# Kernel tuning notes

Hardware: AMD Instinct MI355X
Metric: run time of the kernel (lower is better)

## Reference

```python
import jax, jax.numpy as jnp
import numpy as np

N_NODES = 50000
N_EDGES = 800000
IN_FEATS = 128
OUT_FEATS = 128


def setup_inputs() -> dict:
    key = jax.random.key(0)
    k1, k2, k3, k4 = jax.random.split(key, 4)
    x = jax.random.normal(k1, (N_NODES, IN_FEATS), dtype=jnp.float32)
    src = jax.random.randint(k2, (N_EDGES,), 0, N_NODES, dtype=jnp.int32)
    dst = jax.random.randint(k3, (N_EDGES,), 0, N_NODES, dtype=jnp.int32)
    # xavier_uniform init for weight [in_feats, out_feats]
    limit = float(np.sqrt(6.0 / (IN_FEATS + OUT_FEATS)))
    weight = jax.random.uniform(k4, (IN_FEATS, OUT_FEATS), dtype=jnp.float32,
                                minval=-limit, maxval=limit)
    bias = jnp.zeros((OUT_FEATS,), dtype=jnp.float32)
    return {"x": x, "src": src, "dst": dst, "weight": weight, "bias": bias}


def reference(x, src, dst, weight, bias):
    # GraphConv, norm='both', no edge_weight (copy_u path), single partition:
    #   x <- x * out_deg^{-1/2}
    #   h[v] = sum_{(u->v) in E} x[u]            (SpMM aggregation)
    #   rst = h @ W                               (GEMM)
    #   rst <- rst * in_deg^{-1/2} + bias
    n = x.shape[0]
    ones = jnp.ones(src.shape[0], dtype=x.dtype)
    deg_out = jax.ops.segment_sum(ones, src, num_segments=n)     # [N]
    deg_out = jnp.maximum(deg_out, 1.0)[:, None]                  # clamp(min=1)
    xn = x * jax.lax.rsqrt(deg_out)                               # left norm
    h = jax.ops.segment_sum(xn[src], dst, num_segments=n)        # [N, in]
    rst = h @ weight                                              # [N, out]
    deg_in = jax.ops.segment_sum(ones, dst, num_segments=n)      # [N]
    deg_in = jnp.maximum(deg_in, 1.0)[:, None]
    rst = rst * jax.lax.rsqrt(deg_in)                             # right norm
    return rst + bias
```

## Files before the change

### kernel.cpp

```cpp
#include <hip/hip_runtime.h>

#define F 128
#define RANGE 12500
#define WT_LD 136

typedef unsigned short ushort_t;
typedef _Float16 half8 __attribute__((ext_vector_type(8)));
typedef float f32x4 __attribute__((ext_vector_type(4)));

__device__ inline float bf_lo(unsigned u) { return __uint_as_float(u << 16); }
__device__ inline float bf_hi(unsigned u) { return __uint_as_float(u & 0xffff0000u); }
__device__ inline ushort_t f2bf(float f) {
    unsigned u = __float_as_uint(f);
    return (ushort_t)((u + 0x7fff + ((u >> 16) & 1)) >> 16);
}

__global__ __launch_bounds__(256)
void hist_both_kernel(const int* __restrict__ src, const int* __restrict__ dst,
                      int* __restrict__ part, int E, int S, int SLICE) {
    __shared__ int h[RANGE];
    int b = blockIdx.x, t = threadIdx.x;
    int r = b / S, s = b % S;
    int lo = r * RANGE;
    for (int i = t; i < RANGE; i += 256) h[i] = 0;
    __syncthreads();
    int e0 = s * SLICE, e1 = min(e0 + SLICE, E);
    int e = e0 + t * 4;
    for (; e + 3 < e1; e += 1024) {
        int4 vs4 = *(const int4*)(src + e);
        int4 vd4 = *(const int4*)(dst + e);
        int vs, vd;
        vs = vs4.x - lo; if ((unsigned)vs < (unsigned)RANGE) atomicAdd(&h[vs], 1);
        vs = vs4.y - lo; if ((unsigned)vs < (unsigned)RANGE) atomicAdd(&h[vs], 1);
        vs = vs4.z - lo; if ((unsigned)vs < (unsigned)RANGE) atomicAdd(&h[vs], 1);
        vs = vs4.w - lo; if ((unsigned)vs < (unsigned)RANGE) atomicAdd(&h[vs], 1);
        vd = vd4.x - lo; if ((unsigned)vd < (unsigned)RANGE) atomicAdd(&h[vd], 0x10000);
        vd = vd4.y - lo; if ((unsigned)vd < (unsigned)RANGE) atomicAdd(&h[vd], 0x10000);
        vd = vd4.z - lo; if ((unsigned)vd < (unsigned)RANGE) atomicAdd(&h[vd], 0x10000);
        vd = vd4.w - lo; if ((unsigned)vd < (unsigned)RANGE) atomicAdd(&h[vd], 0x10000);
    }
    for (; e < e1; ++e) {
        int vs = src[e] - lo;
        int vd = dst[e] - lo;
        if ((unsigned)vs < (unsigned)RANGE) atomicAdd(&h[vs], 1);
        if ((unsigned)vd < (unsigned)RANGE) atomicAdd(&h[vd], 0x10000);
    }
    __syncthreads();
    int* outp = part + (size_t)b * RANGE;
    for (int i = t; i < RANGE; i += 256) outp[i] = h[i];
}

__global__ __launch_bounds__(256)
void reduce_all_kernel(const int* __restrict__ part, ushort_t* __restrict__ pre16,
                       float* __restrict__ inv_out, int* __restrict__ cnt_in,
                       int* __restrict__ psum, int S, int N) {
    int b = blockIdx.x, t = threadIdx.x;
    int v = b * 256 + t;
    int run = 0;
    if (v < N) {
        int r = v / RANGE, vp = v % RANGE;
        const int* p = part + (size_t)r * S * RANGE + vp;
        ushort_t* q = pre16 + (size_t)r * S * RANGE + vp;
        int sum_s = 0;
        for (int s = 0; s < S; ++s) {
            int tv = p[(size_t)s * RANGE];
            sum_s += tv & 0xffff;
            q[(size_t)s * RANGE] = (ushort_t)run;
            run += (tv >> 16);
        }
        inv_out[v] = rsqrtf(fmaxf((float)sum_s, 1.0f));
        cnt_in[v] = run;
    }
    int bl = run;
    #pragma unroll
    for (int off = 32; off > 0; off >>= 1) bl += __shfl_down(bl, off);
    __shared__ int ws[4];
    int lane = t & 63, w = t >> 6;
    if (lane == 0) ws[w] = bl;
    __syncthreads();
    if (t == 0) psum[b] = ws[0] + ws[1] + ws[2] + ws[3];
}

__global__ __launch_bounds__(256)
void scan_rows_kernel(const int* __restrict__ cnt_in, const int* __restrict__ psum,
                      int* __restrict__ row_off, int N, int E, int NP) {
    int b = blockIdx.x, t = threadIdx.x;
    int pv = (t < 4 * b && t < NP) ? psum[t] : 0;
    #pragma unroll
    for (int off = 32; off > 0; off >>= 1) pv += __shfl_down(pv, off);
    __shared__ int red[4];
    int lane = t & 63, w = t >> 6;
    if (lane == 0) red[w] = pv;
    if (b == 0 && t == 0) row_off[N] = E;
    __syncthreads();
    int base = red[0] + red[1] + red[2] + red[3];

    int i0 = b * 1024 + t * 4;
    int v[4]; int s = 0;
    #pragma unroll
    for (int j = 0; j < 4; ++j) { int i = i0 + j; v[j] = (i < N) ? cnt_in[i] : 0; s += v[j]; }
    int incl = s;
    #pragma unroll
    for (int off = 1; off < 64; off <<= 1) {
        int u = __shfl_up(incl, off);
        if (lane >= off) incl += u;
    }
    __shared__ int wsum[4];
    if (lane == 63) wsum[w] = incl;
    __syncthreads();
    int wbase = 0;
    #pragma unroll
    for (int j = 0; j < 4; ++j) if (j < w) wbase += wsum[j];
    int run = base + wbase + (incl - s);
    #pragma unroll
    for (int j = 0; j < 4; ++j) {
        int i = i0 + j;
        if (i < N) { row_off[i] = run; run += v[j]; }
    }
}

__global__ __launch_bounds__(256)
void fill_kernel(const int* __restrict__ src, const int* __restrict__ dst,
                 const int* __restrict__ row_off, const ushort_t* __restrict__ pre16,
                 ushort_t* __restrict__ csr_src, int E, int S, int SLICE, int N) {
    __shared__ int cur[RANGE];
    int b = blockIdx.x, t = threadIdx.x;
    int r = b / S, s = b % S;
    int lo = r * RANGE;
    int hi = min(lo + RANGE, N);
    const ushort_t* pp = pre16 + (size_t)b * RANGE;
    for (int i = t; i < hi - lo; i += 256) cur[i] = row_off[lo + i] + pp[i];
    __syncthreads();
    int e0 = s * SLICE, e1 = min(e0 + SLICE, E);
    int e = e0 + t * 4;
    for (; e + 3 < e1; e += 1024) {
        int4 vd4 = *(const int4*)(dst + e);
        int4 vs4 = *(const int4*)(src + e);
        int d;
        d = vd4.x - lo; if ((unsigned)d < (unsigned)(hi - lo)) { int pos = atomicAdd(&cur[d], 1); csr_src[pos] = (ushort_t)vs4.x; }
        d = vd4.y - lo; if ((unsigned)d < (unsigned)(hi - lo)) { int pos = atomicAdd(&cur[d], 1); csr_src[pos] = (ushort_t)vs4.y; }
        d = vd4.z - lo; if ((unsigned)d < (unsigned)(hi - lo)) { int pos = atomicAdd(&cur[d], 1); csr_src[pos] = (ushort_t)vs4.z; }
        d = vd4.w - lo; if ((unsigned)d < (unsigned)(hi - lo)) { int pos = atomicAdd(&cur[d], 1); csr_src[pos] = (ushort_t)vs4.w; }
    }
    for (; e < e1; ++e) {
        int d = dst[e] - lo;
        if ((unsigned)d < (unsigned)(hi - lo)) {
            int pos = atomicAdd(&cur[d], 1);
            csr_src[pos] = (ushort_t)src[e];
        }
    }
}

__global__ __launch_bounds__(256)
void gemm_kernel(const float* __restrict__ x, const float* __restrict__ W,
                 const float* __restrict__ inv_out, ushort_t* __restrict__ Y, int N) {
    __shared__ _Float16 Wt[128 * WT_LD];
    const int t = threadIdx.x;
    for (int i = t; i < 128 * 128; i += 256) {
        int k = i >> 7, c = i & 127;
        Wt[c * WT_LD + k] = (_Float16)W[i];
    }
    __syncthreads();

    const int wv = t >> 6;
    const int l  = t & 63;
    const int m  = l & 15;
    const int q  = l >> 4;
    const int r0w = blockIdx.x * 64 + wv * 16;
    const int rowload = min(r0w + m, N - 1);
    const float* xr = x + (size_t)rowload * F;

    f32x4 acc[8] = {};
    #pragma unroll
    for (int k0 = 0; k0 < 128; k0 += 32) {
        const int kk = k0 + q * 8;
        float4 xa = *(const float4*)(xr + kk);
        float4 xb = *(const float4*)(xr + kk + 4);
        half8 a;
        a[0] = (_Float16)xa.x; a[1] = (_Float16)xa.y;
        a[2] = (_Float16)xa.z; a[3] = (_Float16)xa.w;
        a[4] = (_Float16)xb.x; a[5] = (_Float16)xb.y;
        a[6] = (_Float16)xb.z; a[7] = (_Float16)xb.w;
        #pragma unroll
        for (int ct = 0; ct < 8; ++ct) {
            half8 bfr = *(const half8*)&Wt[(ct * 16 + m) * WT_LD + kk];
            acc[ct] = __builtin_amdgcn_mfma_f32_16x16x32_f16(a, bfr, acc[ct], 0, 0, 0);
        }
    }

    float sc[4]; int rvalid[4];
    #pragma unroll
    for (int reg = 0; reg < 4; ++reg) {
        int rr = r0w + q * 4 + reg;
        rvalid[reg] = rr < N;
        sc[reg] = inv_out[min(rr, N - 1)];
    }
    #pragma unroll
    for (int ct = 0; ct < 8; ++ct) {
        #pragma unroll
        for (int reg = 0; reg < 4; ++reg) {
            if (rvalid[reg]) {
                int rr = r0w + q * 4 + reg;
                Y[(size_t)rr * F + ct * 16 + m] = f2bf(acc[ct][reg] * sc[reg]);
            }
        }
    }
}

__global__ __launch_bounds__(256)
void gather_kernel(const ushort_t* __restrict__ Y, const ushort_t* __restrict__ csr_src,
                   const int* __restrict__ row_off, const float* __restrict__ bias,
                   float* __restrict__ out, int N) {
    int v = blockIdx.x * 4 + (threadIdx.x >> 6);
    if (v >= N) return;
    int lane = threadIdx.x & 63;
    int q = lane >> 4;
    int l16 = lane & 15;
    int beg = row_off[v], end = row_off[v + 1];
    float aA[8] = {0,0,0,0,0,0,0,0};
    float aB[8] = {0,0,0,0,0,0,0,0};
    float aC[8] = {0,0,0,0,0,0,0,0};
    float aD[8] = {0,0,0,0,0,0,0,0};
    int j = beg + q;
    for (; j + 12 < end; j += 16) {
        int s0 = csr_src[j];
        int s1 = csr_src[j + 4];
        int s2 = csr_src[j + 8];
        int s3 = csr_src[j + 12];
        uint4 u0 = *(const uint4*)(Y + (size_t)s0 * F + l16 * 8);
        uint4 u1 = *(const uint4*)(Y + (size_t)s1 * F + l16 * 8);
        uint4 u2 = *(const uint4*)(Y + (size_t)s2 * F + l16 * 8);
        uint4 u3 = *(const uint4*)(Y + (size_t)s3 * F + l16 * 8);
        aA[0] += bf_lo(u0.x); aA[1] += bf_hi(u0.x);
        aA[2] += bf_lo(u0.y); aA[3] += bf_hi(u0.y);
        aA[4] += bf_lo(u0.z); aA[5] += bf_hi(u0.z);
        aA[6] += bf_lo(u0.w); aA[7] += bf_hi(u0.w);
        aB[0] += bf_lo(u1.x); aB[1] += bf_hi(u1.x);
        aB[2] += bf_lo(u1.y); aB[3] += bf_hi(u1.y);
        aB[4] += bf_lo(u1.z); aB[5] += bf_hi(u1.z);
        aB[6] += bf_lo(u1.w); aB[7] += bf_hi(u1.w);
        aC[0] += bf_lo(u2.x); aC[1] += bf_hi(u2.x);
        aC[2] += bf_lo(u2.y); aC[3] += bf_hi(u2.y);
        aC[4] += bf_lo(u2.z); aC[5] += bf_hi(u2.z);
        aC[6] += bf_lo(u2.w); aC[7] += bf_hi(u2.w);
        aD[0] += bf_lo(u3.x); aD[1] += bf_hi(u3.x);
        aD[2] += bf_lo(u3.y); aD[3] += bf_hi(u3.y);
        aD[4] += bf_lo(u3.z); aD[5] += bf_hi(u3.z);
        aD[6] += bf_lo(u3.w); aD[7] += bf_hi(u3.w);
    }
    for (; j < end; j += 4) {
        int s0 = csr_src[j];
        uint4 u0 = *(const uint4*)(Y + (size_t)s0 * F + l16 * 8);
        aA[0] += bf_lo(u0.x); aA[1] += bf_hi(u0.x);
        aA[2] += bf_lo(u0.y); aA[3] += bf_hi(u0.y);
        aA[4] += bf_lo(u0.z); aA[5] += bf_hi(u0.z);
        aA[6] += bf_lo(u0.w); aA[7] += bf_hi(u0.w);
    }
    #pragma unroll
    for (int i = 0; i < 8; ++i) {
        float a = (aA[i] + aB[i]) + (aC[i] + aD[i]);
        a += __shfl_xor(a, 16);
        a += __shfl_xor(a, 32);
        aA[i] = a;
    }
    if (q == 0) {
        float invd = rsqrtf(fmaxf((float)(end - beg), 1.0f));
        float4 b0 = *(const float4*)(bias + l16 * 8);
        float4 b1 = *(const float4*)(bias + l16 * 8 + 4);
        float4 o0, o1;
        o0.x = aA[0] * invd + b0.x; o0.y = aA[1] * invd + b0.y;
        o0.z = aA[2] * invd + b0.z; o0.w = aA[3] * invd + b0.w;
        o1.x = aA[4] * invd + b1.x; o1.y = aA[5] * invd + b1.y;
        o1.z = aA[6] * invd + b1.z; o1.w = aA[7] * invd + b1.w;
        *(float4*)(out + (size_t)v * F + l16 * 8) = o0;
        *(float4*)(out + (size_t)v * F + l16 * 8 + 4) = o1;
    }
}

extern "C" void kernel_launch(void* const* d_in, const int* in_sizes, int n_in,
                              void* d_out, int out_size, void* d_ws, size_t ws_size,
                              hipStream_t stream) {
    const float* x    = (const float*)d_in[0];
    const int*   src  = (const int*)d_in[1];
    const int*   dst  = (const int*)d_in[2];
    const float* W    = (const float*)d_in[3];
    const float* bias = (const float*)d_in[4];
    float* out = (float*)d_out;

    const int N = in_sizes[0] / F;
    const int E = in_sizes[1];
    const int NB = (N + 1023) / 1024;
    const int NP = (N + 255) / 256;
    const int R = (N + RANGE - 1) / RANGE;

    size_t fixed_words = (size_t)N + (size_t)(N + 1) + (size_t)N + (size_t)NP
                       + (size_t)(E + 1) / 2 + 128
                       + ((size_t)N * F + 1) / 2 + 128;
    int S = 64;
    while (S > 2 && (fixed_words + (size_t)R * S * RANGE * 3 / 2) * 4 > ws_size) S >>= 1;
    const int SLICE = (E + S - 1) / S;

    int*   part    = (int*)d_ws;
    int*   cnt_in  = part + (size_t)R * S * RANGE;
    int*   row_off = cnt_in + N;
    float* inv_out = (float*)(row_off + N + 1);
    int*   psum    = (int*)(inv_out + N);
    size_t off_w   = ((size_t)(psum + NP - (int*)d_ws) + 63) & ~(size_t)63;
    ushort_t* csr_src = (ushort_t*)((int*)d_ws + off_w);
    size_t off_w2  = (off_w + ((size_t)E + 1) / 2 + 63) & ~(size_t)63;
    ushort_t* Y    = (ushort_t*)((int*)d_ws + off_w2);
    size_t off_w3  = (off_w2 + ((size_t)N * F + 1) / 2 + 63) & ~(size_t)63;
    ushort_t* pre16 = (ushort_t*)((int*)d_ws + off_w3);

    const int hgrid = R * S;

    hist_both_kernel<<<hgrid, 256, 0, stream>>>(src, dst, part, E, S, SLICE);
    reduce_all_kernel<<<NP, 256, 0, stream>>>(part, pre16, inv_out, cnt_in, psum, S, N);
    scan_rows_kernel<<<NB, 256, 0, stream>>>(cnt_in, psum, row_off, N, E, NP);
    fill_kernel<<<hgrid, 256, 0, stream>>>(src, dst, row_off, pre16, csr_src, E, S, SLICE, N);
    gemm_kernel<<<(N + 63) / 64, 256, 0, stream>>>(x, W, inv_out, Y, N);
    gather_kernel<<<(N + 3) / 4, 256, 0, stream>>>(Y, csr_src, row_off, bias, out, N);
}
```

Before: 174.9 us.

## Replace sliced shared-memory histograms with global atomics and fuse CSR fill into GEMM

Replaces the partitioned shared-memory histogram, reduce and per-slice prefix pipeline with one global-atomic degree kernel, a single scan kernel that also computes the out-degree norms, and a CSR fill that runs as extra blocks of the GEMM launch. The fill increments the row offsets in place, so the gather reads the row end from ro[v] and the row start from ro[v-1]. This removes the large per-slice partial buffers, the extra passes over them and two launches, and lets the scatter overlap the GEMM. In exchange it relies on global atomics with no ordering within a row, and the gather tail now handles up to three leftover edges per lane group.

Result: slower. 250.6 us (+43.3%).

```diff
diff --git a/kernel.cpp b/kernel.cpp
--- a/kernel.cpp
+++ b/kernel.cpp
@@ -1,7 +1,6 @@
 #include <hip/hip_runtime.h>
 
 #define F 128
-#define RANGE 12500
 #define WT_LD 136
 
 typedef unsigned short ushort_t;
@@ -16,89 +15,77 @@
 }
 
 __global__ __launch_bounds__(256)
-void hist_both_kernel(const int* __restrict__ src, const int* __restrict__ dst,
-                      int* __restrict__ part, int E, int S, int SLICE) {
-    __shared__ int h[RANGE];
+void zero_kernel(int* __restrict__ deg, int N) {
+    int i = (blockIdx.x * 256 + threadIdx.x) * 4;
+    if (i + 3 < N) {
+        *(int4*)(deg + i) = make_int4(0, 0, 0, 0);
+    } else {
+        for (; i < N; ++i) deg[i] = 0;
+    }
+}
+
+__global__ __launch_bounds__(256)
+void deg_kernel(const int* __restrict__ src, const int* __restrict__ dst,
+                int* __restrict__ deg, int E) {
+    int i = (blockIdx.x * 256 + threadIdx.x) * 4;
+    if (i + 3 < E) {
+        int4 s4 = *(const int4*)(src + i);
+        int4 d4 = *(const int4*)(dst + i);
+        atomicAdd(&deg[s4.x], 1);
+        atomicAdd(&deg[s4.y], 1);
+        atomicAdd(&deg[s4.z], 1);
+        atomicAdd(&deg[s4.w], 1);
+        atomicAdd(&deg[d4.x], 0x10000);
+        atomicAdd(&deg[d4.y], 0x10000);
+        atomicAdd(&deg[d4.z], 0x10000);
+        atomicAdd(&deg[d4.w], 0x10000);
+    } else {
+        for (; i < E; ++i) {
+            atomicAdd(&deg[src[i]], 1);
+            atomicAdd(&deg[dst[i]], 0x10000);
+        }
+    }
+}
+
+__global__ __launch_bounds__(256)
+void scan_kernel(const int* __restrict__ deg, float* __restrict__ inv_out,
+                 int* __restrict__ ro, int N) {
     int b = blockIdx.x, t = threadIdx.x;
-    int r = b / S, s = b % S;
-    int lo = r * RANGE;
-    for (int i = t; i < RANGE; i += 256) h[i] = 0;
+    int lane = t & 63, w = t >> 6;
+    int lim = b << 10;
+
+    int acc = 0;
+    for (int i = t * 4; i < lim; i += 1024) {
+        int4 d4 = *(const int4*)(deg + i);
+        acc += (int)(((unsigned)d4.x >> 16) + ((unsigned)d4.y >> 16)
+                   + ((unsigned)d4.z >> 16) + ((unsigned)d4.w >> 16));
+    }
+    #pragma unroll
+    for (int off = 32; off > 0; off >>= 1) acc += __shfl_down(acc, off);
+    __shared__ int bsum[4];
+    if (lane == 0) bsum[w] = acc;
     __syncthreads();
-    int e0 = s * SLICE, e1 = min(e0 + SLICE, E);
-    int e = e0 + t * 4;
-    for (; e + 3 < e1; e += 1024) {
-        int4 vs4 = *(const int4*)(src + e);
-        int4 vd4 = *(const int4*)(dst + e);
-        int vs, vd;
-        vs = vs4.x - lo; if ((unsigned)vs < (unsigned)RANGE) atomicAdd(&h[vs], 1);
-        vs = vs4.y - lo; if ((unsigned)vs < (unsigned)RANGE) atomicAdd(&h[vs], 1);
-        vs = vs4.z - lo; if ((unsigned)vs < (unsigned)RANGE) atomicAdd(&h[vs], 1);
-        vs = vs4.w - lo; if ((unsigned)vs < (unsigned)RANGE) atomicAdd(&h[vs], 1);
-        vd = vd4.x - lo; if ((unsigned)vd < (unsigned)RANGE) atomicAdd(&h[vd], 0x10000);
-        vd = vd4.y - lo; if ((unsigned)vd < (unsigned)RANGE) atomicAdd(&h[vd], 0x10000);
-        vd = vd4.z - lo; if ((unsigned)vd < (unsigned)RANGE) atomicAdd(&h[vd], 0x10000);
-        vd = vd4.w - lo; if ((unsigned)vd < (unsigned)RANGE) atomicAdd(&h[vd], 0x10000);
-    }
-    for (; e < e1; ++e) {
-        int vs = src[e] - lo;
-        int vd = dst[e] - lo;
-        if ((unsigned)vs < (unsigned)RANGE) atomicAdd(&h[vs], 1);
-        if ((unsigned)vd < (unsigned)RANGE) atomicAdd(&h[vd], 0x10000);
-    }
-    __syncthreads();
-    int* outp = part + (size_t)b * RANGE;
-    for (int i = t; i < RANGE; i += 256) outp[i] = h[i];
-}
-
-__global__ __launch_bounds__(256)
-void reduce_all_kernel(const int* __restrict__ part, ushort_t* __restrict__ pre16,
-                       float* __restrict__ inv_out, int* __restrict__ cnt_in,
-                       int* __restrict__ psum, int S, int N) {
-    int b = blockIdx.x, t = threadIdx.x;
-    int v = b * 256 + t;
-    int run = 0;
-    if (v < N) {
-        int r = v / RANGE, vp = v % RANGE;
-        const int* p = part + (size_t)r * S * RANGE + vp;
-        ushort_t* q = pre16 + (size_t)r * S * RANGE + vp;
-        int sum_s = 0;
-        for (int s = 0; s < S; ++s) {
-            int tv = p[(size_t)s * RANGE];
-            sum_s += tv & 0xffff;
-            q[(size_t)s * RANGE] = (ushort_t)run;
-            run += (tv >> 16);
-        }
-        inv_out[v] = rsqrtf(fmaxf((float)sum_s, 1.0f));
-        cnt_in[v] = run;
-    }
-    int bl = run;
-    #pragma unroll
-    for (int off = 32; off > 0; off >>= 1) bl += __shfl_down(bl, off);
-    __shared__ int ws[4];
-    int lane = t & 63, w = t >> 6;
-    if (lane == 0) ws[w] = bl;
-    __syncthreads();
-    if (t == 0) psum[b] = ws[0] + ws[1] + ws[2] + ws[3];
-}
-
-__global__ __launch_bounds__(256)
-void scan_rows_kernel(const int* __restrict__ cnt_in, const int* __restrict__ psum,
-                      int* __restrict__ row_off, int N, int E, int NP) {
-    int b = blockIdx.x, t = threadIdx.x;
-    int pv = (t < 4 * b && t < NP) ? psum[t] : 0;
-    #pragma unroll
-    for (int off = 32; off > 0; off >>= 1) pv += __shfl_down(pv, off);
-    __shared__ int red[4];
-    int lane = t & 63, w = t >> 6;
-    if (lane == 0) red[w] = pv;
-    if (b == 0 && t == 0) row_off[N] = E;
-    __syncthreads();
-    int base = red[0] + red[1] + red[2] + red[3];
-
-    int i0 = b * 1024 + t * 4;
-    int v[4]; int s = 0;
-    #pragma unroll
-    for (int j = 0; j < 4; ++j) { int i = i0 + j; v[j] = (i < N) ? cnt_in[i] : 0; s += v[j]; }
+    int base = bsum[0] + bsum[1] + bsum[2] + bsum[3];
+
+    int i0 = lim + t * 4;
+    int v4[4]; int s = 0;
+    if (i0 < N) {
+        int4 d4 = *(const int4*)(deg + i0);
+        v4[0] = (int)((unsigned)d4.x >> 16);
+        v4[1] = (int)((unsigned)d4.y >> 16);
+        v4[2] = (int)((unsigned)d4.z >> 16);
+        v4[3] = (int)((unsigned)d4.w >> 16);
+        s = v4[0] + v4[1] + v4[2] + v4[3];
+        float4 iv;
+        iv.x = rsqrtf(fmaxf((float)(d4.x & 0xffff), 1.0f));
+        iv.y = rsqrtf(fmaxf((float)(d4.y & 0xffff), 1.0f));
+        iv.z = rsqrtf(fmaxf((float)(d4.z & 0xffff), 1.0f));
+        iv.w = rsqrtf(fmaxf((float)(d4.w & 0xffff), 1.0f));
+        *(float4*)(inv_out + i0) = iv;
+    } else {
+        v4[0] = v4[1] = v4[2] = v4[3] = 0;
+    }
+
     int incl = s;
     #pragma unroll
     for (int off = 1; off < 64; off <<= 1) {
@@ -112,50 +99,46 @@
     #pragma unroll
     for (int j = 0; j < 4; ++j) if (j < w) wbase += wsum[j];
     int run = base + wbase + (incl - s);
-    #pragma unroll
-    for (int j = 0; j < 4; ++j) {
-        int i = i0 + j;
-        if (i < N) { row_off[i] = run; run += v[j]; }
-    }
-}
-
-__global__ __launch_bounds__(256)
-void fill_kernel(const int* __restrict__ src, const int* __restrict__ dst,
-                 const int* __restrict__ row_off, const ushort_t* __restrict__ pre16,
-                 ushort_t* __restrict__ csr_src, int E, int S, int SLICE, int N) {
-    __shared__ int cur[RANGE];
-    int b = blockIdx.x, t = threadIdx.x;
-    int r = b / S, s = b % S;
-    int lo = r * RANGE;
-    int hi = min(lo + RANGE, N);
-    const ushort_t* pp = pre16 + (size_t)b * RANGE;
-    for (int i = t; i < hi - lo; i += 256) cur[i] = row_off[lo + i] + pp[i];
-    __syncthreads();
-    int e0 = s * SLICE, e1 = min(e0 + SLICE, E);
-    int e = e0 + t * 4;
-    for (; e + 3 < e1; e += 1024) {
-        int4 vd4 = *(const int4*)(dst + e);
-        int4 vs4 = *(const int4*)(src + e);
-        int d;
-        d = vd4.x - lo; if ((unsigned)d < (unsigned)(hi - lo)) { int pos = atomicAdd(&cur[d], 1); csr_src[pos] = (ushort_t)vs4.x; }
-        d = vd4.y - lo; if ((unsigned)d < (unsigned)(hi - lo)) { int pos = atomicAdd(&cur[d], 1); csr_src[pos] = (ushort_t)vs4.y; }
-        d = vd4.z - lo; if ((unsigned)d < (unsigned)(hi - lo)) { int pos = atomicAdd(&cur[d], 1); csr_src[pos] = (ushort_t)vs4.z; }
-        d = vd4.w - lo; if ((unsigned)d < (unsigned)(hi - lo)) { int pos = atomicAdd(&cur[d], 1); csr_src[pos] = (ushort_t)vs4.w; }
-    }
-    for (; e < e1; ++e) {
-        int d = dst[e] - lo;
-        if ((unsigned)d < (unsigned)(hi - lo)) {
-            int pos = atomicAdd(&cur[d], 1);
-            csr_src[pos] = (ushort_t)src[e];
-        }
-    }
-}
-
-__global__ __launch_bounds__(256)
-void gemm_kernel(const float* __restrict__ x, const float* __restrict__ W,
-                 const float* __restrict__ inv_out, ushort_t* __restrict__ Y, int N) {
+    if (i0 < N) {
+        int4 r4;
+        r4.x = run; run += v4[0];
+        r4.y = run; run += v4[1];
+        r4.z = run; run += v4[2];
+        r4.w = run;
+        *(int4*)(ro + i0) = r4;
+    }
+}
+
+__global__ __launch_bounds__(256)
+void gemm_fill_kernel(const float* __restrict__ x, const float* __restrict__ W,
+                      const float* __restrict__ inv_out, ushort_t* __restrict__ Y,
+                      const int* __restrict__ src, const int* __restrict__ dst,
+                      int* __restrict__ ro, ushort_t* __restrict__ csr,
+                      int N, int E, int FB) {
     __shared__ _Float16 Wt[128 * WT_LD];
     const int t = threadIdx.x;
+    const int blk = blockIdx.x;
+
+    if (blk < FB) {
+        int i = (blk * 256 + t) * 4;
+        if (i + 3 < E) {
+            int4 d4 = *(const int4*)(dst + i);
+            int4 s4 = *(const int4*)(src + i);
+            int p;
+            p = atomicAdd(&ro[d4.x], 1); csr[p] = (ushort_t)s4.x;
+            p = atomicAdd(&ro[d4.y], 1); csr[p] = (ushort_t)s4.y;
+            p = atomicAdd(&ro[d4.z], 1); csr[p] = (ushort_t)s4.z;
+            p = atomicAdd(&ro[d4.w], 1); csr[p] = (ushort_t)s4.w;
+        } else {
+            for (; i < E; ++i) {
+                int p = atomicAdd(&ro[dst[i]], 1);
+                csr[p] = (ushort_t)src[i];
+            }
+        }
+        return;
+    }
+
+    const int gb = blk - FB;
     for (int i = t; i < 128 * 128; i += 256) {
         int k = i >> 7, c = i & 127;
         Wt[c * WT_LD + k] = (_Float16)W[i];
@@ -166,7 +149,7 @@
     const int l  = t & 63;
     const int m  = l & 15;
     const int q  = l >> 4;
-    const int r0w = blockIdx.x * 64 + wv * 16;
+    const int r0w = gb * 64 + wv * 16;
     const int rowload = min(r0w + m, N - 1);
     const float* xr = x + (size_t)rowload * F;
 
@@ -208,25 +191,26 @@
 }
 
 __global__ __launch_bounds__(256)
-void gather_kernel(const ushort_t* __restrict__ Y, const ushort_t* __restrict__ csr_src,
-                   const int* __restrict__ row_off, const float* __restrict__ bias,
+void gather_kernel(const ushort_t* __restrict__ Y, const ushort_t* __restrict__ csr,
+                   const int* __restrict__ ro, const float* __restrict__ bias,
                    float* __restrict__ out, int N) {
     int v = blockIdx.x * 4 + (threadIdx.x >> 6);
     if (v >= N) return;
     int lane = threadIdx.x & 63;
     int q = lane >> 4;
     int l16 = lane & 15;
-    int beg = row_off[v], end = row_off[v + 1];
+    int end = ro[v];
+    int beg = (v == 0) ? 0 : ro[v - 1];
     float aA[8] = {0,0,0,0,0,0,0,0};
     float aB[8] = {0,0,0,0,0,0,0,0};
     float aC[8] = {0,0,0,0,0,0,0,0};
     float aD[8] = {0,0,0,0,0,0,0,0};
     int j = beg + q;
     for (; j + 12 < end; j += 16) {
-        int s0 = csr_src[j];
-        int s1 = csr_src[j + 4];
-        int s2 = csr_src[j + 8];
-        int s3 = csr_src[j + 12];
+        int s0 = csr[j];
+        int s1 = csr[j + 4];
+        int s2 = csr[j + 8];
+        int s3 = csr[j + 12];
         uint4 u0 = *(const uint4*)(Y + (size_t)s0 * F + l16 * 8);
         uint4 u1 = *(const uint4*)(Y + (size_t)s1 * F + l16 * 8);
         uint4 u2 = *(const uint4*)(Y + (size_t)s2 * F + l16 * 8);
@@ -248,13 +232,29 @@
         aD[4] += bf_lo(u3.z); aD[5] += bf_hi(u3.z);
         aD[6] += bf_lo(u3.w); aD[7] += bf_hi(u3.w);
     }
-    for (; j < end; j += 4) {
-        int s0 = csr_src[j];
+    if (j < end) {
+        int s0 = csr[j];
         uint4 u0 = *(const uint4*)(Y + (size_t)s0 * F + l16 * 8);
         aA[0] += bf_lo(u0.x); aA[1] += bf_hi(u0.x);
         aA[2] += bf_lo(u0.y); aA[3] += bf_hi(u0.y);
         aA[4] += bf_lo(u0.z); aA[5] += bf_hi(u0.z);
         aA[6] += bf_lo(u0.w); aA[7] += bf_hi(u0.w);
+    }
+    if (j + 4 < end) {
+        int s1 = csr[j + 4];
+        uint4 u1 = *(const uint4*)(Y + (size_t)s1 * F + l16 * 8);
+        aB[0] += bf_lo(u1.x); aB[1] += bf_hi(u1.x);
+        aB[2] += bf_lo(u1.y); aB[3] += bf_hi(u1.y);
+        aB[4] += bf_lo(u1.z); aB[5] += bf_hi(u1.z);
+        aB[6] += bf_lo(u1.w); aB[7] += bf_hi(u1.w);
+    }
+    if (j + 8 < end) {
+        int s2 = csr[j + 8];
+        uint4 u2 = *(const uint4*)(Y + (size_t)s2 * F + l16 * 8);
+        aC[0] += bf_lo(u2.x); aC[1] += bf_hi(u2.x);
+        aC[2] += bf_lo(u2.y); aC[3] += bf_hi(u2.y);
+        aC[4] += bf_lo(u2.z); aC[5] += bf_hi(u2.z);
+        aC[6] += bf_lo(u2.w); aC[7] += bf_hi(u2.w);
     }
     #pragma unroll
     for (int i = 0; i < 8; ++i) {
@@ -289,35 +289,24 @@
 
     const int N = in_sizes[0] / F;
     const int E = in_sizes[1];
-    const int NB = (N + 1023) / 1024;
-    const int NP = (N + 255) / 256;
-    const int R = (N + RANGE - 1) / RANGE;
-
-    size_t fixed_words = (size_t)N + (size_t)(N + 1) + (size_t)N + (size_t)NP
-                       + (size_t)(E + 1) / 2 + 128
-                       + ((size_t)N * F + 1) / 2 + 128;
-    int S = 64;
-    while (S > 2 && (fixed_words + (size_t)R * S * RANGE * 3 / 2) * 4 > ws_size) S >>= 1;
-    const int SLICE = (E + S - 1) / S;
-
-    int*   part    = (int*)d_ws;
-    int*   cnt_in  = part + (size_t)R * S * RANGE;
-    int*   row_off = cnt_in + N;
-    float* inv_out = (float*)(row_off + N + 1);
-    int*   psum    = (int*)(inv_out + N);
-    size_t off_w   = ((size_t)(psum + NP - (int*)d_ws) + 63) & ~(size_t)63;
-    ushort_t* csr_src = (ushort_t*)((int*)d_ws + off_w);
-    size_t off_w2  = (off_w + ((size_t)E + 1) / 2 + 63) & ~(size_t)63;
-    ushort_t* Y    = (ushort_t*)((int*)d_ws + off_w2);
-    size_t off_w3  = (off_w2 + ((size_t)N * F + 1) / 2 + 63) & ~(size_t)63;
-    ushort_t* pre16 = (ushort_t*)((int*)d_ws + off_w3);
-
-    const int hgrid = R * S;
-
-    hist_both_kernel<<<hgrid, 256, 0, stream>>>(src, dst, part, E, S, SLICE);
-    reduce_all_kernel<<<NP, 256, 0, stream>>>(part, pre16, inv_out, cnt_in, psum, S, N);
-    scan_rows_kernel<<<NB, 256, 0, stream>>>(cnt_in, psum, row_off, N, E, NP);
-    fill_kernel<<<hgrid, 256, 0, stream>>>(src, dst, row_off, pre16, csr_src, E, S, SLICE, N);
-    gemm_kernel<<<(N + 63) / 64, 256, 0, stream>>>(x, W, inv_out, Y, N);
-    gather_kernel<<<(N + 3) / 4, 256, 0, stream>>>(Y, csr_src, row_off, bias, out, N);
-}
+
+    int*   deg     = (int*)d_ws;
+    int*   ro      = deg + N;
+    float* inv_out = (float*)(ro + N);
+    size_t csr_off = (size_t)N * 12;
+    ushort_t* csr  = (ushort_t*)((char*)d_ws + csr_off);
+    size_t y_off   = (csr_off + (size_t)E * 2 + 255) & ~(size_t)255;
+    ushort_t* Y    = (ushort_t*)((char*)d_ws + y_off);
+
+    const int ZB = (N + 1023) / 1024;
+    const int EB = (E + 1023) / 1024;
+    const int SB = (N + 1023) / 1024;
+    const int GB = (N + 63) / 64;
+
+    zero_kernel<<<ZB, 256, 0, stream>>>(deg, N);
+    deg_kernel<<<EB, 256, 0, stream>>>(src, dst, deg, E);
+    scan_kernel<<<SB, 256, 0, stream>>>(deg, inv_out, ro, N);
+    gemm_fill_kernel<<<EB + GB, 256, 0, stream>>>(x, W, inv_out, Y, src, dst,
+                                                  ro, csr, N, E, EB);
+    gather_kernel<<<(N + 3) / 4, 256, 0, stream>>>(Y, csr, ro, bias, out, N);
+}
```

## Merge CSR fill and GEMM into one launch; unroll gather tail

Applied to the files above, without the earlier changes.

The CSR fill kernel and the GEMM kernel are independent, so they are merged into one launch whose first blocks do the fill and whose remaining blocks do the GEMM, with shared memory as a union. This removes one kernel boundary and lets the atomic-bound fill and the MFMA-bound GEMM run at the same time on different CUs. The gather tail loop is replaced by up to three predicated loads feeding separate accumulators, which adds more loads in flight. The union takes the larger of the two shared-memory footprints, which can lower occupancy for the GEMM blocks.

New measurement: 167.0 us. -4.5%, faster.

```diff
diff --git a/kernel.cpp b/kernel.cpp
--- a/kernel.cpp
+++ b/kernel.cpp
@@ -120,45 +120,51 @@
 }
 
 __global__ __launch_bounds__(256)
-void fill_kernel(const int* __restrict__ src, const int* __restrict__ dst,
-                 const int* __restrict__ row_off, const ushort_t* __restrict__ pre16,
-                 ushort_t* __restrict__ csr_src, int E, int S, int SLICE, int N) {
-    __shared__ int cur[RANGE];
-    int b = blockIdx.x, t = threadIdx.x;
-    int r = b / S, s = b % S;
-    int lo = r * RANGE;
-    int hi = min(lo + RANGE, N);
-    const ushort_t* pp = pre16 + (size_t)b * RANGE;
-    for (int i = t; i < hi - lo; i += 256) cur[i] = row_off[lo + i] + pp[i];
-    __syncthreads();
-    int e0 = s * SLICE, e1 = min(e0 + SLICE, E);
-    int e = e0 + t * 4;
-    for (; e + 3 < e1; e += 1024) {
-        int4 vd4 = *(const int4*)(dst + e);
-        int4 vs4 = *(const int4*)(src + e);
-        int d;
-        d = vd4.x - lo; if ((unsigned)d < (unsigned)(hi - lo)) { int pos = atomicAdd(&cur[d], 1); csr_src[pos] = (ushort_t)vs4.x; }
-        d = vd4.y - lo; if ((unsigned)d < (unsigned)(hi - lo)) { int pos = atomicAdd(&cur[d], 1); csr_src[pos] = (ushort_t)vs4.y; }
-        d = vd4.z - lo; if ((unsigned)d < (unsigned)(hi - lo)) { int pos = atomicAdd(&cur[d], 1); csr_src[pos] = (ushort_t)vs4.z; }
-        d = vd4.w - lo; if ((unsigned)d < (unsigned)(hi - lo)) { int pos = atomicAdd(&cur[d], 1); csr_src[pos] = (ushort_t)vs4.w; }
-    }
-    for (; e < e1; ++e) {
-        int d = dst[e] - lo;
-        if ((unsigned)d < (unsigned)(hi - lo)) {
-            int pos = atomicAdd(&cur[d], 1);
-            csr_src[pos] = (ushort_t)src[e];
-        }
-    }
-}
-
-__global__ __launch_bounds__(256)
-void gemm_kernel(const float* __restrict__ x, const float* __restrict__ W,
-                 const float* __restrict__ inv_out, ushort_t* __restrict__ Y, int N) {
-    __shared__ _Float16 Wt[128 * WT_LD];
+void fill_gemm_kernel(const int* __restrict__ src, const int* __restrict__ dst,
+                      const int* __restrict__ row_off, const ushort_t* __restrict__ pre16,
+                      ushort_t* __restrict__ csr_src,
+                      const float* __restrict__ x, const float* __restrict__ W,
+                      const float* __restrict__ inv_out, ushort_t* __restrict__ Y,
+                      int E, int S, int SLICE, int N, int FB) {
+    __shared__ union {
+        int cur[RANGE];
+        _Float16 Wt[128 * WT_LD];
+    } sm;
     const int t = threadIdx.x;
+    const int blk = blockIdx.x;
+
+    if (blk < FB) {
+        int r = blk / S, s = blk % S;
+        int lo = r * RANGE;
+        int hi = min(lo + RANGE, N);
+        const ushort_t* pp = pre16 + (size_t)blk * RANGE;
+        for (int i = t; i < hi - lo; i += 256) sm.cur[i] = row_off[lo + i] + pp[i];
+        __syncthreads();
+        int e0 = s * SLICE, e1 = min(e0 + SLICE, E);
+        int e = e0 + t * 4;
+        for (; e + 3 < e1; e += 1024) {
+            int4 vd4 = *(const int4*)(dst + e);
+            int4 vs4 = *(const int4*)(src + e);
+            int d;
+            d = vd4.x - lo; if ((unsigned)d < (unsigned)(hi - lo)) { int pos = atomicAdd(&sm.cur[d], 1); csr_src[pos] = (ushort_t)vs4.x; }
+            d = vd4.y - lo; if ((unsigned)d < (unsigned)(hi - lo)) { int pos = atomicAdd(&sm.cur[d], 1); csr_src[pos] = (ushort_t)vs4.y; }
+            d = vd4.z - lo; if ((unsigned)d < (unsigned)(hi - lo)) { int pos = atomicAdd(&sm.cur[d], 1); csr_src[pos] = (ushort_t)vs4.z; }
+            d = vd4.w - lo; if ((unsigned)d < (unsigned)(hi - lo)) { int pos = atomicAdd(&sm.cur[d], 1); csr_src[pos] = (ushort_t)vs4.w; }
+        }
+        for (; e < e1; ++e) {
+            int d = dst[e] - lo;
+            if ((unsigned)d < (unsigned)(hi - lo)) {
+                int pos = atomicAdd(&sm.cur[d], 1);
+                csr_src[pos] = (ushort_t)src[e];
+            }
+        }
+        return;
+    }
+
+    const int gb = blk - FB;
     for (int i = t; i < 128 * 128; i += 256) {
         int k = i >> 7, c = i & 127;
-        Wt[c * WT_LD + k] = (_Float16)W[i];
+        sm.Wt[c * WT_LD + k] = (_Float16)W[i];
     }
     __syncthreads();
 
@@ -166,7 +172,7 @@
     const int l  = t & 63;
     const int m  = l & 15;
     const int q  = l >> 4;
-    const int r0w = blockIdx.x * 64 + wv * 16;
+    const int r0w = gb * 64 + wv * 16;
     const int rowload = min(r0w + m, N - 1);
     const float* xr = x + (size_t)rowload * F;
 
@@ -183,7 +189,7 @@
         a[6] = (_Float16)xb.z; a[7] = (_Float16)xb.w;
         #pragma unroll
         for (int ct = 0; ct < 8; ++ct) {
-            half8 bfr = *(const half8*)&Wt[(ct * 16 + m) * WT_LD + kk];
+            half8 bfr = *(const half8*)&sm.Wt[(ct * 16 + m) * WT_LD + kk];
             acc[ct] = __builtin_amdgcn_mfma_f32_16x16x32_f16(a, bfr, acc[ct], 0, 0, 0);
         }
     }
@@ -248,13 +254,29 @@
         aD[4] += bf_lo(u3.z); aD[5] += bf_hi(u3.z);
         aD[6] += bf_lo(u3.w); aD[7] += bf_hi(u3.w);
     }
-    for (; j < end; j += 4) {
+    if (j < end) {
         int s0 = csr_src[j];
         uint4 u0 = *(const uint4*)(Y + (size_t)s0 * F + l16 * 8);
         aA[0] += bf_lo(u0.x); aA[1] += bf_hi(u0.x);
         aA[2] += bf_lo(u0.y); aA[3] += bf_hi(u0.y);
         aA[4] += bf_lo(u0.z); aA[5] += bf_hi(u0.z);
         aA[6] += bf_lo(u0.w); aA[7] += bf_hi(u0.w);
+    }
+    if (j + 4 < end) {
+        int s1 = csr_src[j + 4];
+        uint4 u1 = *(const uint4*)(Y + (size_t)s1 * F + l16 * 8);
+        aB[0] += bf_lo(u1.x); aB[1] += bf_hi(u1.x);
+        aB[2] += bf_lo(u1.y); aB[3] += bf_hi(u1.y);
+        aB[4] += bf_lo(u1.z); aB[5] += bf_hi(u1.z);
+        aB[6] += bf_lo(u1.w); aB[7] += bf_hi(u1.w);
+    }
+    if (j + 8 < end) {
+        int s2 = csr_src[j + 8];
+        uint4 u2 = *(const uint4*)(Y + (size_t)s2 * F + l16 * 8);
+        aC[0] += bf_lo(u2.x); aC[1] += bf_hi(u2.x);
+        aC[2] += bf_lo(u2.y); aC[3] += bf_hi(u2.y);
+        aC[4] += bf_lo(u2.z); aC[5] += bf_hi(u2.z);
+        aC[6] += bf_lo(u2.w); aC[7] += bf_hi(u2.w);
     }
     #pragma unroll
     for (int i = 0; i < 8; ++i) {
@@ -313,11 +335,12 @@
     ushort_t* pre16 = (ushort_t*)((int*)d_ws + off_w3);
 
     const int hgrid = R * S;
+    const int GB = (N + 63) / 64;
 
     hist_both_kernel<<<hgrid, 256, 0, stream>>>(src, dst, part, E, S, SLICE);
     reduce_all_kernel<<<NP, 256, 0, stream>>>(part, pre16, inv_out, cnt_in, psum, S, N);
     scan_rows_kernel<<<NB, 256, 0, stream>>>(cnt_in, psum, row_off, N, E, NP);
-    fill_kernel<<<hgrid, 256, 0, stream>>>(src, dst, row_off, pre16, csr_src, E, S, SLICE, N);
-    gemm_kernel<<<(N + 63) / 64, 256, 0, stream>>>(x, W, inv_out, Y, N);
+    fill_gemm_kernel<<<hgrid + GB, 256, 0, stream>>>(src, dst, row_off, pre16, csr_src,
+                                                     x, W, inv_out, Y, E, S, SLICE, N, hgrid);
     gather_kernel<<<(N + 3) / 4, 256, 0, stream>>>(Y, csr_src, row_off, bias, out, N);
 }
```
